# Kernel optimization log

Hardware: AMD Instinct MI355X
Metric: run time of the kernel (lower is better)

The kernel has to match this reference:

```python
import jax, jax.numpy as jnp
import numpy as np

B, L = 2, 2048
DIM, VOCAB, NL = 1024, 32000, 4
DSTATE, DCONV, EXPAND, HEADDIM = 128, 4, 2, 64
DIN = EXPAND * DIM            # 2048
H = DIN // HEADDIM            # 32 heads
CONVDIM = DIN + 2 * DSTATE    # 2304
DPROJ = 2 * DIN + 2 * DSTATE + H  # 4384
FFN = 4 * DIM                 # 4096
Q = 128                       # SSD chunk size
EPS = 1e-6


def _rms(x):
    return x * jax.lax.rsqrt(jnp.mean(x * x, axis=-1, keepdims=True) + EPS)


def _causal_conv(x, w, b):
    # x [B,L,C], depthwise causal conv, w [C,DCONV], b [C]
    y = jax.lax.conv_general_dilated(
        x.transpose(0, 2, 1), w[:, None, :], (1,), [(DCONV - 1, 0)],
        dimension_numbers=('NCH', 'OIH', 'NCH'), feature_group_count=CONVDIM)
    return (y + b[:, None]).transpose(0, 2, 1)


def _ssd(x, dt, A, Bm, Cm):
    # Exact selective scan h_t = h_{t-1}*exp(dt_t*A) + dt_t * x_t B_t ; y_t = C_t . h_t
    # computed in chunked (SSD) matmul form. x [b,l,h,p], dt [b,l,h], A [h], Bm/Cm [b,l,n]
    b, l, h, p = x.shape
    n = Bm.shape[-1]
    c = l // Q
    xr = x.reshape(b, c, Q, h, p)
    dtr = dt.reshape(b, c, Q, h)
    ar = (dt * A).reshape(b, c, Q, h)          # per-step log-decay (<= 0)
    Br = Bm.reshape(b, c, Q, n)
    Cr = Cm.reshape(b, c, Q, n)
    ca = jnp.cumsum(ar, axis=2)                # inclusive cumulative log-decay
    # ---- intra-chunk: causal decay-weighted 'attention' ----
    cah = ca.transpose(0, 1, 3, 2)             # [b,c,h,Q]
    idx = jnp.arange(Q)
    mask = idx[:, None] >= idx[None, :]
    diff = jnp.where(mask[None, None, None], cah[..., :, None] - cah[..., None, :], -jnp.inf)
    M = jnp.exp(diff)                          # [b,c,h,Q,Q]
    CB = jnp.einsum('bcin,bcjn->bcij', Cr, Br)
    T = CB[:, :, None] * M                     # [b,c,h,Q,Q]
    y_intra = jnp.einsum('bchij,bcjh,bcjhp->bcihp', T, dtr, xr)
    # ---- chunk-final states ----
    w = jnp.exp(ca[:, :, -1:, :] - ca) * dtr   # [b,c,Q,h]
    states = jnp.einsum('bcjh,bcjn,bcjhp->bchpn', w, Br, xr)
    chunk_decay = jnp.exp(ca[:, :, -1, :])     # [b,c,h]
    def step(s, inp):
        cd, st = inp
        prev = s
        s = s * cd[:, :, None, None] + st
        return s, prev
    s0 = jnp.zeros((b, h, p, n), x.dtype)
    _, s_prev = jax.lax.scan(step, s0, (chunk_decay.transpose(1, 0, 2),
                                        states.transpose(1, 0, 2, 3, 4)))
    s_prev = s_prev.transpose(1, 0, 2, 3, 4)   # [b,c,h,p,n] state entering each chunk
    y_inter = jnp.einsum('bcih,bcin,bchpn->bcihp', jnp.exp(ca), Cr, s_prev)
    return (y_intra + y_inter).reshape(b, l, h, p)


def _mamba(x, Wi, cw, cb, dtb, Alog, Dp, nw, Wo):
    bsz, sl, _ = x.shape
    zxbcdt = x @ Wi.T                          # [b,l,DPROJ]
    z = zxbcdt[..., :DIN]
    xBC = zxbcdt[..., DIN:DIN + CONVDIM]
    dtraw = zxbcdt[..., DIN + CONVDIM:]
    xBC = jax.nn.silu(_causal_conv(xBC, cw, cb))
    xs = xBC[..., :DIN]
    Bm = xBC[..., DIN:DIN + DSTATE]
    Cm = xBC[..., DIN + DSTATE:]
    dt = jax.nn.softplus(dtraw + dtb)
    A = -jnp.exp(Alog)
    x4 = xs.reshape(bsz, sl, H, HEADDIM)
    y = _ssd(x4, dt, A, Bm, Cm) + Dp[None, None, :, None] * x4
    y = y.reshape(bsz, sl, DIN)
    yg = y * jax.nn.silu(z)                    # gated RMSNorm (norm_before_gate=False)
    y = _rms(yg) * nw
    return y @ Wo.T


def _forward(tokens, embedding, lm_head_bias, in_proj_w, conv_w, conv_b,
             dt_bias, A_log, D, mnorm_w, out_proj_w, u_w, v_w, o_w):
    x = embedding[tokens]
    for li in range(NL):
        for _ in range(2):  # original applies each (mamba, ffn) pair twice
            x = _rms(x)
            x = x + _mamba(x, in_proj_w[li], conv_w[li], conv_b[li], dt_bias[li],
                           A_log[li], D[li], mnorm_w[li], out_proj_w[li])
            x = _rms(x)
            x = x + ((x @ u_w[li].T) * (x @ v_w[li].T)) @ o_w[li].T  # SGLU, dropout=0
    return x @ embedding.T + lm_head_bias      # tied lm_head


def setup_inputs():
    key = jax.random.key(0)
    ks = jax.random.split(key, 16)
    s = 0.02
    return {
        'tokens': jax.random.randint(ks[0], (B, L), 0, VOCAB),
        'embedding': jax.random.normal(ks[1], (VOCAB, DIM), jnp.float32) * s,
        'lm_head_bias': jnp.zeros((VOCAB,), jnp.float32),
        'in_proj_w': jax.random.normal(ks[2], (NL, DPROJ, DIM), jnp.float32) * s,
        'conv_w': jax.random.normal(ks[3], (NL, CONVDIM, DCONV), jnp.float32) * 0.2,
        'conv_b': jnp.zeros((NL, CONVDIM), jnp.float32),
        'dt_bias': jax.random.normal(ks[4], (NL, H), jnp.float32) * 0.3 - 3.0,
        'A_log': jnp.log(jax.random.uniform(ks[5], (NL, H), jnp.float32, 1.0, 16.0)),
        'D': jnp.ones((NL, H), jnp.float32) + 0.1 * jax.random.normal(ks[6], (NL, H), jnp.float32),
        'mnorm_w': jnp.ones((NL, DIN), jnp.float32),
        'out_proj_w': jax.random.normal(ks[7], (NL, DIM, DIN), jnp.float32) * s,
        'u_w': jax.random.normal(ks[8], (NL, FFN, DIM), jnp.float32) * s,
        'v_w': jax.random.normal(ks[9], (NL, FFN, DIM), jnp.float32) * s,
        'o_w': jax.random.normal(ks[10], (NL, DIM, FFN), jnp.float32) * s,
    }


def reference(tokens, embedding, lm_head_bias, in_proj_w, conv_w, conv_b,
              dt_bias, A_log, D, mnorm_w, out_proj_w, u_w, v_w, o_w):
    return _forward(tokens, embedding, lm_head_bias, in_proj_w, conv_w, conv_b,
                    dt_bias, A_log, D, mnorm_w, out_proj_w, u_w, v_w, o_w)
```

## Files before the change

### kernel.cpp

```cpp
#include <hip/hip_runtime.h>
#include <hip/hip_bf16.h>

#define BSZ 2
#define LSEQ 2048
#define DIM 1024
#define VOCAB 32000
#define NLAYER 4
#define DSTATE 128
#define DCONV 4
#define HEADDIM 64
#define DIN 2048
#define NH 32
#define CONVDIM 2304
#define DPROJ 4384
#define FFN 4096
#define QLEN 128
#define NTOK 4096
#define NCHUNK 32
#define CPB 16
#define DTOFF 4352

#define SMEM_BYTES 147456
#define SMEM2 131072

using f32x4 = __attribute__((ext_vector_type(4))) float;
using f16   = _Float16;
using f16x4 = __attribute__((ext_vector_type(4))) _Float16;
using f16x8 = __attribute__((ext_vector_type(8))) _Float16;

__device__ __forceinline__ void gld16(const void* g, void* l) {
  __builtin_amdgcn_global_load_lds(
      (const __attribute__((address_space(1))) unsigned int*)g,
      (__attribute__((address_space(3))) unsigned int*)l, 16, 0, 0);
}

__device__ __forceinline__ void swz_tiles(int& bx, int& by) {
  const int nx = gridDim.x, ny = gridDim.y;
  const int nwg = nx * ny;
  int bid = blockIdx.y * nx + blockIdx.x;
  if ((nwg & 7) == 0) bid = (bid & 7) * (nwg >> 3) + (bid >> 3);
  const int CW = 8;
  const int nchx = nx / CW;
  const int per = CW * ny;
  const int ch = bid / per;
  if (ch < nchx) {
    int wi = bid - ch * per;
    bx = ch * CW + (wi & (CW - 1));
    by = wi / CW;
  } else {
    int tb = bid - nchx * per;
    int tw = nx - nchx * CW;
    bx = nchx * CW + (tb % tw);
    by = tb / tw;
  }
}

__global__ __launch_bounds__(512, 2) void gemm_p(
    const f16* __restrict__ A, const f16* __restrict__ B,
    f16* __restrict__ Cg, float* __restrict__ dtr,
    int N, int Ksub, int lda, int ldb, int ldc)
{
  extern __shared__ char smem[];
  const int tid  = threadIdx.x;
  const int lane = tid & 63;
  const int wid  = tid >> 6;
  int bx, by; swz_tiles(bx, by);
  const int m0 = by * 256;
  const int n0 = bx * 128;
  const size_t kbase = (size_t)blockIdx.z * Ksub;
  if (gridDim.z > 1) Cg += (size_t)blockIdx.z * (size_t)gridDim.y * 256 * ldc;
  const int NT = Ksub >> 6;

  int arA[4], acA[4];
#pragma unroll
  for (int L = 0; L < 4; ++L) {
    int q = L * 512 + tid;
    int row = q >> 3;
    arA[L] = m0 + row;
    acA[L] = ((q & 7) ^ (row & 7)) << 3;
  }
  int brB[2], bcB[2];
#pragma unroll
  for (int L = 0; L < 2; ++L) {
    int q = L * 512 + tid;
    int row = q >> 3;
    int r = n0 + row; if (r > N - 1) r = N - 1;
    brB[L] = r;
    bcB[L] = ((q & 7) ^ (row & 7)) << 3;
  }

  auto stage = [&](int tt) {
    const int b = tt - (tt / 3) * 3;
    char* Ad = smem + b * 32768;
    char* Bd = smem + 98304 + b * 16384;
    const int kb = tt << 6;
#pragma unroll
    for (int L = 0; L < 4; ++L)
      gld16(A + (size_t)arA[L] * lda + kbase + kb + acA[L], Ad + (L * 512 + tid) * 16);
#pragma unroll
    for (int L = 0; L < 2; ++L)
      gld16(B + (size_t)brB[L] * ldb + kbase + kb + bcB[L], Bd + (L * 512 + tid) * 16);
  };

  const int wm = (wid >> 1) << 6;
  const int wn = (wid & 1) << 6;
  const int fr = lane & 15;
  const int kg = lane >> 4;

  f32x4 acc[4][4] = {};

  stage(0);
  stage(1);

  for (int t = 0; t < NT; ++t) {
    const int b = t - (t / 3) * 3;
    if (t + 2 < NT) {
      stage(t + 2);
      asm volatile("s_waitcnt vmcnt(12)" ::: "memory");
    } else if (t + 1 < NT) {
      asm volatile("s_waitcnt vmcnt(6)" ::: "memory");
    } else {
      asm volatile("s_waitcnt vmcnt(0)" ::: "memory");
    }
    __builtin_amdgcn_s_barrier();
    asm volatile("" ::: "memory");
    const f16* Ab = (const f16*)(smem + b * 32768);
    const f16* Bb = (const f16*)(smem + 98304 + b * 16384);
#pragma unroll
    for (int s = 0; s < 2; ++s) {
      f16x8 af[4], bf[4];
#pragma unroll
      for (int j = 0; j < 4; ++j) {
        int row = wm + j * 16 + fr;
        int g = kg + s * 4;
        af[j] = *(const f16x8*)&Ab[row * 64 + ((g ^ (row & 7)) << 3)];
      }
#pragma unroll
      for (int i = 0; i < 4; ++i) {
        int row = wn + i * 16 + fr;
        int g = kg + s * 4;
        bf[i] = *(const f16x8*)&Bb[row * 64 + ((g ^ (row & 7)) << 3)];
      }
      __builtin_amdgcn_s_setprio(1);
#pragma unroll
      for (int i = 0; i < 4; ++i)
#pragma unroll
        for (int j = 0; j < 4; ++j)
          acc[i][j] = __builtin_amdgcn_mfma_f32_16x16x32_f16(bf[i], af[j], acc[i][j], 0, 0, 0);
      __builtin_amdgcn_s_setprio(0);
    }
    asm volatile("" ::: "memory");
    __builtin_amdgcn_s_barrier();
    asm volatile("" ::: "memory");
  }

  const int c4 = kg << 2;
#pragma unroll
  for (int i = 0; i < 4; ++i) {
    const int col = n0 + wn + i * 16 + c4;
    if (col >= N) continue;
#pragma unroll
    for (int j = 0; j < 4; ++j) {
      const int row = m0 + wm + j * 16 + fr;
      f16x4 h;
#pragma unroll
      for (int r = 0; r < 4; ++r) h[r] = (f16)acc[i][j][r];
      *(f16x4*)(Cg + (size_t)row * ldc + col) = h;
      if (dtr && col >= DTOFF)
        *(f32x4*)(dtr + (size_t)row * NH + (col - DTOFF)) = acc[i][j];
    }
  }
}

__global__ __launch_bounds__(512, 2) void gemm_p2(
    const f16* __restrict__ A, const f16* __restrict__ B,
    float* __restrict__ Cf, const float* __restrict__ bias,
    int N, int Ksub, int lda, int ldb, int ldc)
{
  extern __shared__ char smem[];
  const int tid  = threadIdx.x;
  const int lane = tid & 63;
  const int wid  = tid >> 6;
  int bx, by; swz_tiles(bx, by);
  const int m0 = by * 256;
  const int n0 = bx * 256;
  const size_t kbase = (size_t)blockIdx.z * Ksub;
  const int NT = Ksub >> 6;

  int arA[4], acA[4], brB[4], bcB[4];
#pragma unroll
  for (int L = 0; L < 4; ++L) {
    int q = L * 512 + tid;
    int row = q >> 3;
    arA[L] = m0 + row;
    acA[L] = ((q & 7) ^ (row & 7)) << 3;
    int r = n0 + row; if (r > N - 1) r = N - 1;
    brB[L] = r;
    bcB[L] = acA[L];
  }

  auto stage = [&](int tt) {
    const int b = tt & 1;
    char* Ad = smem + b * 65536;
    char* Bd = Ad + 32768;
    const int kb = tt << 6;
#pragma unroll
    for (int L = 0; L < 4; ++L)
      gld16(A + (size_t)arA[L] * lda + kbase + kb + acA[L], Ad + (L * 512 + tid) * 16);
#pragma unroll
    for (int L = 0; L < 4; ++L)
      gld16(B + (size_t)brB[L] * ldb + kbase + kb + bcB[L], Bd + (L * 512 + tid) * 16);
  };

  const int wm = (wid >> 2) << 7;
  const int wn = (wid & 3) << 6;
  const int fr = lane & 15;
  const int kg = lane >> 4;

  f32x4 acc[4][8] = {};

  stage(0);

  for (int t = 0; t < NT; ++t) {
    if (t + 1 < NT) {
      stage(t + 1);
      asm volatile("s_waitcnt vmcnt(8)" ::: "memory");
    } else {
      asm volatile("s_waitcnt vmcnt(0)" ::: "memory");
    }
    __builtin_amdgcn_s_barrier();
    asm volatile("" ::: "memory");
    const f16* Ab = (const f16*)(smem + (t & 1) * 65536);
    const f16* Bb = Ab + 16384;
#pragma unroll
    for (int s = 0; s < 2; ++s) {
      const int g = kg + s * 4;
      f16x8 af[8], bf[4];
#pragma unroll
      for (int j = 0; j < 8; ++j) {
        int row = wm + j * 16 + fr;
        af[j] = *(const f16x8*)&Ab[row * 64 + ((g ^ (row & 7)) << 3)];
      }
#pragma unroll
      for (int i = 0; i < 4; ++i) {
        int row = wn + i * 16 + fr;
        bf[i] = *(const f16x8*)&Bb[row * 64 + ((g ^ (row & 7)) << 3)];
      }
      __builtin_amdgcn_s_setprio(1);
#pragma unroll
      for (int i = 0; i < 4; ++i)
#pragma unroll
        for (int j = 0; j < 8; ++j)
          acc[i][j] = __builtin_amdgcn_mfma_f32_16x16x32_f16(bf[i], af[j], acc[i][j], 0, 0, 0);
      __builtin_amdgcn_s_setprio(0);
    }
    asm volatile("" ::: "memory");
    __builtin_amdgcn_s_barrier();
    asm volatile("" ::: "memory");
  }

  const int c4 = kg << 2;
#pragma unroll
  for (int i = 0; i < 4; ++i) {
    const int col = n0 + wn + i * 16 + c4;
    if (col >= N) continue;
    f32x4 bv = bias ? *(const f32x4*)(bias + col) : f32x4{0, 0, 0, 0};
#pragma unroll
    for (int j = 0; j < 8; ++j) {
      const int row = m0 + wm + j * 16 + fr;
      *(f32x4*)(Cf + (size_t)row * ldc + col) = acc[i][j] + bv;
    }
  }
}

__global__ __launch_bounds__(512, 2) void gemm_uv2(
    const f16* __restrict__ A, const f16* __restrict__ Bu, const f16* __restrict__ Bv,
    f16* __restrict__ Gh)
{
  extern __shared__ char smem[];
  const int tid  = threadIdx.x;
  const int lane = tid & 63;
  const int wid  = tid >> 6;
  int bx, by; swz_tiles(bx, by);
  const int m0 = by * 256;
  const int n0 = bx * 128;
  const int NT = DIM >> 6;

  int arA[4], acA[4];
  const f16* bp[4];
  int bcB[4];
#pragma unroll
  for (int L = 0; L < 4; ++L) {
    int q = L * 512 + tid;
    int row = q >> 3;
    arA[L] = m0 + row;
    acA[L] = ((q & 7) ^ (row & 7)) << 3;
    bcB[L] = acA[L];
    bp[L] = (row < 128) ? (Bu + (size_t)(n0 + row) * DIM)
                        : (Bv + (size_t)(n0 + row - 128) * DIM);
  }

  auto stage = [&](int tt) {
    const int b = tt & 1;
    char* Ad = smem + b * 65536;
    char* Bd = Ad + 32768;
    const int kb = tt << 6;
#pragma unroll
    for (int L = 0; L < 4; ++L)
      gld16(A + (size_t)arA[L] * DIM + kb + acA[L], Ad + (L * 512 + tid) * 16);
#pragma unroll
    for (int L = 0; L < 4; ++L)
      gld16(bp[L] + kb + bcB[L], Bd + (L * 512 + tid) * 16);
  };

  const int wm = (wid >> 1) << 6;
  const int wn = (wid & 1) << 6;
  const int fr = lane & 15;
  const int kg = lane >> 4;

  f32x4 accu[4][4] = {}, accv[4][4] = {};

  stage(0);

  for (int t = 0; t < NT; ++t) {
    if (t + 1 < NT) {
      stage(t + 1);
      asm volatile("s_waitcnt vmcnt(8)" ::: "memory");
    } else {
      asm volatile("s_waitcnt vmcnt(0)" ::: "memory");
    }
    __builtin_amdgcn_s_barrier();
    asm volatile("" ::: "memory");
    const f16* Ab = (const f16*)(smem + (t & 1) * 65536);
    const f16* Bb = Ab + 16384;
#pragma unroll
    for (int s = 0; s < 2; ++s) {
      const int g = kg + s * 4;
      f16x8 af[4], bfu[4], bfv[4];
#pragma unroll
      for (int j = 0; j < 4; ++j) {
        int row = wm + j * 16 + fr;
        af[j] = *(const f16x8*)&Ab[row * 64 + ((g ^ (row & 7)) << 3)];
      }
#pragma unroll
      for (int i = 0; i < 4; ++i) {
        int ru = wn + i * 16 + fr;
        int rv = 128 + wn + i * 16 + fr;
        bfu[i] = *(const f16x8*)&Bb[ru * 64 + ((g ^ (ru & 7)) << 3)];
        bfv[i] = *(const f16x8*)&Bb[rv * 64 + ((g ^ (rv & 7)) << 3)];
      }
      __builtin_amdgcn_s_setprio(1);
#pragma unroll
      for (int i = 0; i < 4; ++i)
#pragma unroll
        for (int j = 0; j < 4; ++j) {
          accu[i][j] = __builtin_amdgcn_mfma_f32_16x16x32_f16(bfu[i], af[j], accu[i][j], 0, 0, 0);
          accv[i][j] = __builtin_amdgcn_mfma_f32_16x16x32_f16(bfv[i], af[j], accv[i][j], 0, 0, 0);
        }
      __builtin_amdgcn_s_setprio(0);
    }
    asm volatile("" ::: "memory");
    __builtin_amdgcn_s_barrier();
    asm volatile("" ::: "memory");
  }

  const int c4 = kg << 2;
#pragma unroll
  for (int i = 0; i < 4; ++i) {
    const int col = n0 + wn + i * 16 + c4;
#pragma unroll
    for (int j = 0; j < 4; ++j) {
      const int row = m0 + wm + j * 16 + fr;
      f16x4 h;
#pragma unroll
      for (int r = 0; r < 4; ++r)
        h[r] = (f16)(accu[i][j][r] * accv[i][j][r]);
      *(f16x4*)(Gh + (size_t)row * FFN + col) = h;
    }
  }
}

template <bool DORMS>
__global__ __launch_bounds__(256) void reduce_rms(const f16* __restrict__ parts,
                                                  const float* __restrict__ resid,
                                                  float* __restrict__ xn,
                                                  f16* __restrict__ outh, int np)
{
  const int row = blockIdx.x, tid = threadIdx.x;
  const size_t base = (size_t)row * DIM + tid * 4;
  f32x4 s = *(const f32x4*)(resid + base);
  for (int p = 0; p < np; ++p) {
    f16x4 pv = *(const f16x4*)(parts + (size_t)p * (NTOK * DIM) + base);
#pragma unroll
    for (int c = 0; c < 4; ++c) s[c] += (float)pv[c];
  }
  if constexpr (!DORMS) {
    f16x4 h;
#pragma unroll
    for (int c = 0; c < 4; ++c) h[c] = (f16)s[c];
    *(f16x4*)(outh + base) = h;
    return;
  }
  float ss = s[0] * s[0] + s[1] * s[1] + s[2] * s[2] + s[3] * s[3];
  for (int o = 32; o; o >>= 1) ss += __shfl_down(ss, o);
  __shared__ float red[4];
  if ((tid & 63) == 0) red[tid >> 6] = ss;
  __syncthreads();
  ss = red[0] + red[1] + red[2] + red[3];
  const float sc = rsqrtf(ss * (1.f / 1024.f) + 1e-6f);
  f32x4 o4 = s * sc;
  *(f32x4*)(xn + base) = o4;
  f16x4 h;
#pragma unroll
  for (int c = 0; c < 4; ++c) h[c] = (f16)o4[c];
  *(f16x4*)(outh + base) = h;
}

__global__ __launch_bounds__(256) void cvt_f2h_k(const float* __restrict__ src,
                                                 f16* __restrict__ dst, int n)
{
  for (size_t i = ((size_t)blockIdx.x * 256 + threadIdx.x) * 4; i < (size_t)n;
       i += (size_t)gridDim.x * 1024) {
    f32x4 v = *(const f32x4*)(src + i);
    f16x4 o;
#pragma unroll
    for (int c = 0; c < 4; ++c) o[c] = (f16)v[c];
    *(f16x4*)(dst + i) = o;
  }
}

__global__ __launch_bounds__(256) void cvt_wts(
    const float* __restrict__ inw, const float* __restrict__ outw,
    const float* __restrict__ uw, const float* __restrict__ vw,
    const float* __restrict__ ow,
    f16* __restrict__ w_in, f16* __restrict__ w_out,
    f16* __restrict__ w_uv, f16* __restrict__ w_o)
{
  const int b = blockIdx.x;
  const float* src; f16* dst;
  if (b < 17536) {
    int li = b / 4384, ib = b - li * 4384;
    src = inw  + (size_t)li * 4489216 + (size_t)ib * 1024;
    dst = w_in + (size_t)li * 4489216 + (size_t)ib * 1024;
  } else if (b < 25728) {
    int lb = b - 17536, li = lb >> 11, ib = lb & 2047;
    src = outw  + (size_t)li * 2097152 + (size_t)ib * 1024;
    dst = w_out + (size_t)li * 2097152 + (size_t)ib * 1024;
  } else if (b < 42112) {
    int lb = b - 25728, li = lb >> 12, ib = lb & 4095;
    src = uw   + (size_t)li * 4194304 + (size_t)ib * 1024;
    dst = w_uv + (size_t)li * 8388608 + (size_t)ib * 1024;
  } else if (b < 58496) {
    int lb = b - 42112, li = lb >> 12, ib = lb & 4095;
    src = vw   + (size_t)li * 4194304 + (size_t)ib * 1024;
    dst = w_uv + (size_t)li * 8388608 + 4194304 + (size_t)ib * 1024;
  } else {
    int lb = b - 58496, li = lb >> 12, ib = lb & 4095;
    src = ow  + (size_t)li * 4194304 + (size_t)ib * 1024;
    dst = w_o + (size_t)li * 4194304 + (size_t)ib * 1024;
  }
  const size_t i = (size_t)threadIdx.x * 4;
  f32x4 v = *(const f32x4*)(src + i);
  f16x4 o;
#pragma unroll
  for (int c = 0; c < 4; ++c) o[c] = (f16)v[c];
  *(f16x4*)(dst + i) = o;
}

__global__ __launch_bounds__(256) void gather_k(const int* __restrict__ tok,
                                                const float* __restrict__ emb,
                                                float* __restrict__ x)
{
  const int row = blockIdx.x;
  const int t = tok[row];
  const f32x4* s = (const f32x4*)(emb + (size_t)t * DIM);
  f32x4* d = (f32x4*)(x + (size_t)row * DIM);
  d[threadIdx.x] = s[threadIdx.x];
}

__global__ __launch_bounds__(256) void rms1024(const float* __restrict__ in,
                                               float* __restrict__ outf,
                                               f16* __restrict__ outh)
{
  const int row = blockIdx.x, tid = threadIdx.x;
  f32x4 v = ((const f32x4*)(in + (size_t)row * DIM))[tid];
  float ss = v[0] * v[0] + v[1] * v[1] + v[2] * v[2] + v[3] * v[3];
  for (int o = 32; o; o >>= 1) ss += __shfl_down(ss, o);
  __shared__ float red[4];
  if ((tid & 63) == 0) red[tid >> 6] = ss;
  __syncthreads();
  ss = red[0] + red[1] + red[2] + red[3];
  const float sc = rsqrtf(ss * (1.f / 1024.f) + 1e-6f);
  f32x4 o4 = v * sc;
  ((f32x4*)(outf + (size_t)row * DIM))[tid] = o4;
  f16x4 h;
#pragma unroll
  for (int c = 0; c < 4; ++c) h[c] = (f16)o4[c];
  ((f16x4*)(outh + (size_t)row * DIM))[tid] = h;
}

__global__ __launch_bounds__(256) void convdt(const f16* __restrict__ zx,
                                              const float* __restrict__ dtrw,
                                              const float* __restrict__ cw,
                                              const float* __restrict__ cbias,
                                              const float* __restrict__ dtb,
                                              const float* __restrict__ alog,
                                              f16* __restrict__ xbc,
                                              float* __restrict__ dt,
                                              float* __restrict__ ca)
{
  if (blockIdx.x < 576) {
    const int sid = blockIdx.x * 256 + threadIdx.x;
    const int c0 = (sid % 576) * 4;
    const int t0 = (sid / 576) * 16;
    float w[4][4], bs[4];
#pragma unroll
    for (int cc = 0; cc < 4; ++cc) {
      f32x4 wv = *(const f32x4*)(cw + (size_t)(c0 + cc) * 4);
      w[cc][0] = wv[0]; w[cc][1] = wv[1]; w[cc][2] = wv[2]; w[cc][3] = wv[3];
      bs[cc] = cbias[c0 + cc];
    }
    const int l0 = t0 & (LSEQ - 1);
    float x3[4] = {}, x2[4] = {}, x1[4] = {};
    if (l0 != 0) {
      f16x4 a = *(const f16x4*)(zx + (size_t)(t0 - 3) * DPROJ + DIN + c0);
      f16x4 b = *(const f16x4*)(zx + (size_t)(t0 - 2) * DPROJ + DIN + c0);
      f16x4 d = *(const f16x4*)(zx + (size_t)(t0 - 1) * DPROJ + DIN + c0);
#pragma unroll
      for (int c = 0; c < 4; ++c) { x3[c] = (float)a[c]; x2[c] = (float)b[c]; x1[c] = (float)d[c]; }
    }
    for (int i = 0; i < 16; ++i) {
      const int t = t0 + i;
      f16x4 xcv = *(const f16x4*)(zx + (size_t)t * DPROJ + DIN + c0);
      f16x4 o;
#pragma unroll
      for (int cc = 0; cc < 4; ++cc) {
        float xc = (float)xcv[cc];
        float a = bs[cc] + x3[cc] * w[cc][0] + x2[cc] * w[cc][1] +
                  x1[cc] * w[cc][2] + xc * w[cc][3];
        o[cc] = (f16)(a / (1.f + expf(-a)));
        x3[cc] = x2[cc]; x2[cc] = x1[cc]; x1[cc] = xc;
      }
      *(f16x4*)(xbc + (size_t)t * CONVDIM + c0) = o;
    }
  } else {
    const int loc = (threadIdx.x >> 7) * 128;
    const int u = (blockIdx.x - 576) * 2 + (threadIdx.x >> 7);
    const int bc = u >> 5, h = u & 31, q = threadIdx.x & 127;
    const int t = bc * 128 + q;
    float raw = dtrw[(size_t)t * NH + h] + dtb[h];
    float d = raw > 20.f ? raw : log1pf(expf(raw));
    dt[t * 32 + h] = d;
    float a = -expf(alog[h]) * d;
    __shared__ float s[256];
    s[loc + q] = a;
    __syncthreads();
    for (int off = 1; off < 128; off <<= 1) {
      float v = (q >= off) ? s[loc + q - off] : 0.f;
      __syncthreads();
      s[loc + q] += v;
      __syncthreads();
    }
    ca[(size_t)u * 128 + q] = s[loc + q];
  }
}

__global__ __launch_bounds__(256) void cb_mfma(const f16* __restrict__ xbc,
                                               float* __restrict__ CBo)
{
  const int bc = blockIdx.x;
  __shared__ f16 Cm[128 * 72], Bm[128 * 72];
  const int tid = threadIdx.x, lane = tid & 63, wid = tid >> 6;
  const int fr = lane & 15, kg = lane >> 4;
  f32x4 acc[2][8] = {};
  const int i = tid & 127;
  const f16* rowp = xbc + (size_t)(bc * 128 + i) * CONVDIM + DIN;

  for (int kh = 0; kh < 2; ++kh) {
#pragma unroll
    for (int it = 0; it < 8; ++it) {
      int idx = it * 256 + tid;
      int n0 = (idx >> 7) * 4;
      *(f16x4*)&Bm[i * 72 + n0] = *(const f16x4*)(rowp + kh * 64 + n0);
      *(f16x4*)&Cm[i * 72 + n0] = *(const f16x4*)(rowp + DSTATE + kh * 64 + n0);
    }
    __syncthreads();
#pragma unroll
    for (int kf = 0; kf < 2; ++kf) {
      const int ko = kf * 32 + kg * 8;
      f16x8 cf[2], bf[8];
#pragma unroll
      for (int ii = 0; ii < 2; ++ii)
        cf[ii] = *(const f16x8*)&Cm[((wid * 2 + ii) * 16 + fr) * 72 + ko];
#pragma unroll
      for (int jj = 0; jj < 8; ++jj)
        bf[jj] = *(const f16x8*)&Bm[(jj * 16 + fr) * 72 + ko];
      __builtin_amdgcn_s_setprio(1);
#pragma unroll
      for (int ii = 0; ii < 2; ++ii)
#pragma unroll
        for (int jj = 0; jj < 8; ++jj)
          acc[ii][jj] = __builtin_amdgcn_mfma_f32_16x16x32_f16(cf[ii], bf[jj], acc[ii][jj], 0, 0, 0);
      __builtin_amdgcn_s_setprio(0);
    }
    __syncthreads();
  }
  float* out = CBo + (size_t)bc * 16384;
#pragma unroll
  for (int ii = 0; ii < 2; ++ii) {
    const int i0 = (wid * 2 + ii) * 16 + kg * 4;
#pragma unroll
    for (int jj = 0; jj < 8; ++jj) {
      const int j = jj * 16 + fr;
#pragma unroll
      for (int r = 0; r < 4; ++r)
        out[(size_t)(i0 + r) * 128 + j] = acc[ii][jj][r];
    }
  }
}

__global__ __launch_bounds__(256) void ssd_states(const f16* __restrict__ xbc,
                                                  const float* __restrict__ dt,
                                                  const float* __restrict__ ca,
                                                  float* __restrict__ ST)
{
  const int bc = blockIdx.x >> 5, h = blockIdx.x & 31;
  __shared__ f16 Am[128 * 136];
  __shared__ f16 Bm[64 * 136];
  __shared__ float warr[128];
  const int tid = threadIdx.x, lane = tid & 63, wid = tid >> 6;
  if (tid < 128) {
    float cv = ca[(size_t)blockIdx.x * 128 + tid];
    float cl = ca[(size_t)blockIdx.x * 128 + 127];
    warr[tid] = expf(cl - cv) * dt[(size_t)(bc * 128 + tid) * 32 + h];
  }
  __syncthreads();
  {
    const int j = tid & 127;
    const float wj = warr[j];
    const f16* br = xbc + (size_t)(bc * 128 + j) * CONVDIM + DIN;
#pragma unroll
    for (int it = 0; it < 16; ++it) {
      int idx = it * 256 + tid;
      int n0 = (idx >> 7) * 4;
      f16x4 v = *(const f16x4*)(br + n0);
#pragma unroll
      for (int c = 0; c < 4; ++c) Am[(n0 + c) * 136 + j] = (f16)((float)v[c] * wj);
    }
    const f16* xr = xbc + (size_t)(bc * 128 + j) * CONVDIM + h * 64;
#pragma unroll
    for (int it = 0; it < 8; ++it) {
      int idx = it * 256 + tid;
      int p0 = (idx >> 7) * 4;
      f16x4 v = *(const f16x4*)(xr + p0);
#pragma unroll
      for (int c = 0; c < 4; ++c) Bm[(p0 + c) * 136 + j] = v[c];
    }
  }
  __syncthreads();
  const int fr = lane & 15, kg = lane >> 4;
  f32x4 acc[2][4] = {};
#pragma unroll
  for (int kf = 0; kf < 4; ++kf) {
    const int ko = kf * 32 + kg * 8;
    f16x8 bw[2], xf[4];
#pragma unroll
    for (int ii = 0; ii < 2; ++ii)
      bw[ii] = *(const f16x8*)&Am[((wid * 2 + ii) * 16 + fr) * 136 + ko];
#pragma unroll
    for (int pi = 0; pi < 4; ++pi)
      xf[pi] = *(const f16x8*)&Bm[(pi * 16 + fr) * 136 + ko];
    __builtin_amdgcn_s_setprio(1);
#pragma unroll
    for (int ii = 0; ii < 2; ++ii)
#pragma unroll
      for (int pi = 0; pi < 4; ++pi)
        acc[ii][pi] = __builtin_amdgcn_mfma_f32_16x16x32_f16(bw[ii], xf[pi], acc[ii][pi], 0, 0, 0);
    __builtin_amdgcn_s_setprio(0);
  }
  float* sb = ST + (size_t)blockIdx.x * 8192;
#pragma unroll
  for (int ii = 0; ii < 2; ++ii) {
    const int n0 = (wid * 2 + ii) * 16 + kg * 4;
#pragma unroll
    for (int pi = 0; pi < 4; ++pi) {
      const int p = pi * 16 + fr;
      *(f32x4*)(sb + (size_t)p * 128 + n0) = acc[ii][pi];
    }
  }
}

__global__ __launch_bounds__(256) void scan_k(const float* __restrict__ ca,
                                              float* __restrict__ states)
{
  const int b = blockIdx.x >> 10, h = (blockIdx.x >> 5) & 31, seg = blockIdx.x & 31;
  const int e = seg * 256 + threadIdx.x;
  float s = 0.f;
  for (int c = 0; c < CPB; ++c) {
    int bc = b * CPB + c;
    float cd = expf(ca[(size_t)(bc * 32 + h) * 128 + 127]);
    size_t idx = (size_t)(bc * 32 + h) * 8192 + e;
    float v = states[idx];
    states[idx] = s;
    s = s * cd + v;
  }
}

__global__ __launch_bounds__(256) void ssd_y(const f16* __restrict__ xbc,
                                             const float* __restrict__ dt,
                                             const float* __restrict__ ca,
                                             const float* __restrict__ CB,
                                             const float* __restrict__ Dvec,
                                             const float* __restrict__ ST,
                                             f16* __restrict__ ybuf)
{
  const int bc = blockIdx.x >> 5, h = blockIdx.x & 31;
  __shared__ f16 Am[128 * 136];
  __shared__ f16 Bm[64 * 136];
  __shared__ float cas[128], dtl[128];
  const int tid = threadIdx.x, lane = tid & 63, wid = tid >> 6;
  if (tid < 128) {
    cas[tid] = ca[(size_t)blockIdx.x * 128 + tid];
    dtl[tid] = dt[(size_t)(bc * 128 + tid) * 32 + h];
  }
  __syncthreads();
  {
    const int j = tid & 127;
    const float dj = dtl[j];
    const f16* xr = xbc + (size_t)(bc * 128 + j) * CONVDIM + h * 64;
#pragma unroll
    for (int it = 0; it < 8; ++it) {
      int idx = it * 256 + tid;
      int p0 = (idx >> 7) * 4;
      f16x4 v = *(const f16x4*)(xr + p0);
#pragma unroll
      for (int c = 0; c < 4; ++c) Bm[(p0 + c) * 136 + j] = (f16)((float)v[c] * dj);
    }
  }
  {
    const int i = tid >> 1;
    const int jh = (tid & 1) * 64;
    const float cai = cas[i];
    const float* cbr = CB + (size_t)bc * 16384 + (size_t)i * 128 + jh;
#pragma unroll
    for (int g = 0; g < 8; ++g) {
      int j0 = g * 8;
      f32x4 v0 = *(const f32x4*)(cbr + j0);
      f32x4 v1 = *(const f32x4*)(cbr + j0 + 4);
      f16x8 tv;
#pragma unroll
      for (int c = 0; c < 8; ++c) {
        int j = jh + j0 + c;
        float cbv = (c < 4) ? v0[c] : v1[c - 4];
        float val = (j <= i) ? cbv * expf(cai - cas[j]) : 0.f;
        tv[c] = (f16)val;
      }
      *(f16x8*)&Am[i * 136 + jh + j0] = tv;
    }
  }
  __syncthreads();
  const int fr = lane & 15, kg = lane >> 4;
  f32x4 a1[2][4] = {}, a2[2][4] = {};
#pragma unroll
  for (int kf = 0; kf < 4; ++kf) {
    const int ko = kf * 32 + kg * 8;
    f16x8 xf[4], tf[2];
#pragma unroll
    for (int pi = 0; pi < 4; ++pi)
      xf[pi] = *(const f16x8*)&Bm[(pi * 16 + fr) * 136 + ko];
#pragma unroll
    for (int ii = 0; ii < 2; ++ii)
      tf[ii] = *(const f16x8*)&Am[((wid * 2 + ii) * 16 + fr) * 136 + ko];
    __builtin_amdgcn_s_setprio(1);
#pragma unroll
    for (int ii = 0; ii < 2; ++ii)
#pragma unroll
      for (int pi = 0; pi < 4; ++pi)
        a1[ii][pi] = __builtin_amdgcn_mfma_f32_16x16x32_f16(xf[pi], tf[ii], a1[ii][pi], 0, 0, 0);
    __builtin_amdgcn_s_setprio(0);
  }
  __syncthreads();
  {
    const int i = tid & 127;
    const f16* cr = xbc + (size_t)(bc * 128 + i) * CONVDIM + DIN + DSTATE;
#pragma unroll
    for (int it = 0; it < 16; ++it) {
      int idx = it * 256 + tid;
      int n0 = (idx >> 7) * 4;
      *(f16x4*)&Am[i * 136 + n0] = *(const f16x4*)(cr + n0);
    }
    const float* sr = ST + (size_t)blockIdx.x * 8192;
    const int p = tid & 63;
#pragma unroll
    for (int it = 0; it < 8; ++it) {
      int idx = it * 256 + tid;
      int n0 = (idx >> 6) * 4;
      f32x4 v = *(const f32x4*)(sr + (size_t)p * 128 + n0);
      f16x4 hv;
#pragma unroll
      for (int c = 0; c < 4; ++c) hv[c] = (f16)v[c];
      *(f16x4*)&Bm[p * 136 + n0] = hv;
    }
  }
  __syncthreads();
#pragma unroll
  for (int kf = 0; kf < 4; ++kf) {
    const int ko = kf * 32 + kg * 8;
    f16x8 sf[4], cf[2];
#pragma unroll
    for (int pi = 0; pi < 4; ++pi)
      sf[pi] = *(const f16x8*)&Bm[(pi * 16 + fr) * 136 + ko];
#pragma unroll
    for (int ii = 0; ii < 2; ++ii)
      cf[ii] = *(const f16x8*)&Am[((wid * 2 + ii) * 16 + fr) * 136 + ko];
    __builtin_amdgcn_s_setprio(1);
#pragma unroll
    for (int ii = 0; ii < 2; ++ii)
#pragma unroll
      for (int pi = 0; pi < 4; ++pi)
        a2[ii][pi] = __builtin_amdgcn_mfma_f32_16x16x32_f16(sf[pi], cf[ii], a2[ii][pi], 0, 0, 0);
    __builtin_amdgcn_s_setprio(0);
  }
  const float dh = Dvec[h];
#pragma unroll
  for (int ii = 0; ii < 2; ++ii) {
    const int i = (wid * 2 + ii) * 16 + fr;
    const float ei = expf(cas[i]);
    const int tg = bc * 128 + i;
#pragma unroll
    for (int pi = 0; pi < 4; ++pi) {
      const int p0 = pi * 16 + kg * 4;
      f16x4 xv = *(const f16x4*)(xbc + (size_t)tg * CONVDIM + h * 64 + p0);
      f16x4 yo;
#pragma unroll
      for (int r = 0; r < 4; ++r)
        yo[r] = (f16)(a1[ii][pi][r] + ei * a2[ii][pi][r] + dh * (float)xv[r]);
      *(f16x4*)(ybuf + (size_t)tg * DIN + h * 64 + p0) = yo;
    }
  }
}

__global__ __launch_bounds__(256) void gate_rms(const f16* __restrict__ ybuf,
                                                const f16* __restrict__ zx,
                                                const float* __restrict__ nw,
                                                f16* __restrict__ outh)
{
  const int row = blockIdx.x, tid = threadIdx.x;
  f16x8 yv = *(const f16x8*)(ybuf + (size_t)row * DIN + tid * 8);
  f16x8 zv = *(const f16x8*)(zx + (size_t)row * DPROJ + tid * 8);
  float g[8];
  float ss = 0.f;
#pragma unroll
  for (int c = 0; c < 8; ++c) {
    float z = (float)zv[c];
    g[c] = (float)yv[c] * (z / (1.f + expf(-z)));
    ss += g[c] * g[c];
  }
  for (int o = 32; o; o >>= 1) ss += __shfl_down(ss, o);
  __shared__ float red[4];
  if ((tid & 63) == 0) red[tid >> 6] = ss;
  __syncthreads();
  ss = red[0] + red[1] + red[2] + red[3];
  const float sc = rsqrtf(ss * (1.f / 2048.f) + 1e-6f);
  f32x4 w0 = *(const f32x4*)(nw + tid * 8);
  f32x4 w1 = *(const f32x4*)(nw + tid * 8 + 4);
  f16x8 h;
#pragma unroll
  for (int c = 0; c < 8; ++c) {
    float w = (c < 4) ? w0[c] : w1[c - 4];
    h[c] = (f16)(g[c] * sc * w);
  }
  *(f16x8*)(outh + (size_t)row * DIN + tid * 8) = h;
}

extern "C" void kernel_launch(void* const* d_in, const int* in_sizes, int n_in,
                              void* d_out, int out_size, void* d_ws, size_t ws_size,
                              hipStream_t stream)
{
  (void)in_sizes; (void)n_in; (void)out_size; (void)ws_size;
  const int*   tokens = (const int*)d_in[0];
  const float* emb    = (const float*)d_in[1];
  const float* lmb    = (const float*)d_in[2];
  const float* inw    = (const float*)d_in[3];
  const float* cw     = (const float*)d_in[4];
  const float* cbias  = (const float*)d_in[5];
  const float* dtb    = (const float*)d_in[6];
  const float* alog   = (const float*)d_in[7];
  const float* Dvec   = (const float*)d_in[8];
  const float* nw     = (const float*)d_in[9];
  const float* outw   = (const float*)d_in[10];
  const float* uw     = (const float*)d_in[11];
  const float* vw     = (const float*)d_in[12];
  const float* ow     = (const float*)d_in[13];

  char* ws = (char*)d_ws;
  size_t off = 0;
  auto alloc = [&](size_t bytes) { void* p = ws + off; off += (bytes + 255) & ~(size_t)255; return p; };
  f16* emb_h   = (f16*)alloc((size_t)VOCAB * DIM * 2);
  float* xbuf  = (float*)alloc((size_t)NTOK * DIM * 4);
  float* xn    = (float*)alloc((size_t)NTOK * DIM * 4);
  f16* xnh     = (f16*)alloc((size_t)NTOK * DIM * 2);
  f16* xh_lm   = (f16*)alloc((size_t)NTOK * DIM * 2);
  float* dtraw = (float*)alloc((size_t)NTOK * NH * 4);
  float* dtbuf = (float*)alloc((size_t)NTOK * NH * 4);
  float* cabuf = (float*)alloc((size_t)NCHUNK * NH * QLEN * 4);
  float* CBbuf = (float*)alloc((size_t)NCHUNK * QLEN * QLEN * 4);
  f16* abh     = (f16*)alloc((size_t)NTOK * FFN * 2);

  char* ob = (char*)d_out;
  float* states = (float*)(ob);
  f16* zxb      = (f16*)(ob + 40000000);
  f16* xbc      = (f16*)(ob + 80000000);
  f16* ybuf     = (f16*)(ob + 100000000);
  f16* parts    = (f16*)(ob + 120000000);
  f16* w_in     = (f16*)(ob + 160000000);
  f16* w_out    = (f16*)(ob + 196000000);
  f16* w_uv     = (f16*)(ob + 213000000);
  f16* w_o      = (f16*)(ob + 281000000);

  cvt_f2h_k<<<4096, 256, 0, stream>>>(emb, emb_h, VOCAB * DIM);
  cvt_wts<<<74880, 256, 0, stream>>>(inw, outw, uw, vw, ow, w_in, w_out, w_uv, w_o);
  gather_k<<<NTOK, 256, 0, stream>>>(tokens, emb, xbuf);
  rms1024<<<NTOK, 256, 0, stream>>>(xbuf, xn, xnh);

  for (int it = 0; it < 2 * NLAYER; ++it) {
    const int li = it >> 1;
    const f16* w_inL  = w_in  + (size_t)li * 4489216;
    const f16* w_outL = w_out + (size_t)li * 2097152;
    const f16* w_uL   = w_uv  + (size_t)li * 8388608;
    const f16* w_vL   = w_uL  + 4194304;
    const f16* w_oL   = w_o   + (size_t)li * 4194304;
    gemm_p<<<dim3((DPROJ + 127) / 128, NTOK / 256, 1), 512, SMEM_BYTES, stream>>>(
        xnh, w_inL, zxb, dtraw, DPROJ, DIM, DIM, DIM, DPROJ);
    convdt<<<1088, 256, 0, stream>>>(zxb, dtraw, cw + (size_t)li * CONVDIM * DCONV,
                                     cbias + (size_t)li * CONVDIM,
                                     dtb + li * NH, alog + li * NH, xbc, dtbuf, cabuf);
    cb_mfma<<<NCHUNK, 256, 0, stream>>>(xbc, CBbuf);
    ssd_states<<<NCHUNK * NH, 256, 0, stream>>>(xbc, dtbuf, cabuf, states);
    scan_k<<<2048, 256, 0, stream>>>(cabuf, states);
    ssd_y<<<NCHUNK * NH, 256, 0, stream>>>(xbc, dtbuf, cabuf, CBbuf,
                                           Dvec + li * NH, states, ybuf);
    gate_rms<<<NTOK, 256, 0, stream>>>(ybuf, zxb, nw + (size_t)li * DIN, abh);
    gemm_p<<<dim3(DIM / 128, NTOK / 256, 2), 512, SMEM_BYTES, stream>>>(
        abh, w_outL, parts, nullptr, DIM, DIN / 2, DIN, DIN, DIM);
    reduce_rms<true><<<NTOK, 256, 0, stream>>>(parts, xn, xn, xnh, 2);
    gemm_uv2<<<dim3(FFN / 128, NTOK / 256, 1), 512, SMEM2, stream>>>(
        xnh, w_uL, w_vL, abh);
    gemm_p<<<dim3(DIM / 128, NTOK / 256, 2), 512, SMEM_BYTES, stream>>>(
        abh, w_oL, parts, nullptr, DIM, FFN / 2, FFN, FFN, DIM);
    if (it < 2 * NLAYER - 1)
      reduce_rms<true><<<NTOK, 256, 0, stream>>>(parts, xn, xn, xnh, 2);
    else
      reduce_rms<false><<<NTOK, 256, 0, stream>>>(parts, xn, nullptr, xh_lm, 2);
  }

  gemm_p2<<<dim3(VOCAB / 256, NTOK / 256, 1), 512, SMEM2, stream>>>(
      xh_lm, emb_h, (float*)d_out, lmb, VOCAB, DIM, DIM, DIM, VOCAB);
}
```

Measured before the change: 3.165 ms.

## Use one barrier per k-step in gemm_p and reuse it for LM head

```diff
diff --git a/kernel.cpp b/kernel.cpp
--- a/kernel.cpp
+++ b/kernel.cpp
@@ -55,9 +55,11 @@
   }
 }
 
+template <int MODE>
 __global__ __launch_bounds__(512, 2) void gemm_p(
     const f16* __restrict__ A, const f16* __restrict__ B,
-    f16* __restrict__ Cg, float* __restrict__ dtr,
+    f16* __restrict__ Cg, float* __restrict__ Cf,
+    float* __restrict__ dtr, const float* __restrict__ bias,
     int N, int Ksub, int lda, int ldb, int ldc)
 {
   extern __shared__ char smem[];
@@ -114,16 +116,14 @@
 
   for (int t = 0; t < NT; ++t) {
     const int b = t - (t / 3) * 3;
-    if (t + 2 < NT) {
-      stage(t + 2);
-      asm volatile("s_waitcnt vmcnt(12)" ::: "memory");
-    } else if (t + 1 < NT) {
+    if (t + 1 < NT) {
       asm volatile("s_waitcnt vmcnt(6)" ::: "memory");
     } else {
       asm volatile("s_waitcnt vmcnt(0)" ::: "memory");
     }
     __builtin_amdgcn_s_barrier();
     asm volatile("" ::: "memory");
+    if (t + 2 < NT) stage(t + 2);
     const f16* Ab = (const f16*)(smem + b * 32768);
     const f16* Bb = (const f16*)(smem + 98304 + b * 16384);
 #pragma unroll
@@ -150,8 +150,6 @@
       __builtin_amdgcn_s_setprio(0);
     }
     asm volatile("" ::: "memory");
-    __builtin_amdgcn_s_barrier();
-    asm volatile("" ::: "memory");
   }
 
   const int c4 = kg << 2;
@@ -162,113 +160,17 @@
 #pragma unroll
     for (int j = 0; j < 4; ++j) {
       const int row = m0 + wm + j * 16 + fr;
-      f16x4 h;
-#pragma unroll
-      for (int r = 0; r < 4; ++r) h[r] = (f16)acc[i][j][r];
-      *(f16x4*)(Cg + (size_t)row * ldc + col) = h;
-      if (dtr && col >= DTOFF)
-        *(f32x4*)(dtr + (size_t)row * NH + (col - DTOFF)) = acc[i][j];
-    }
-  }
-}
-
-__global__ __launch_bounds__(512, 2) void gemm_p2(
-    const f16* __restrict__ A, const f16* __restrict__ B,
-    float* __restrict__ Cf, const float* __restrict__ bias,
-    int N, int Ksub, int lda, int ldb, int ldc)
-{
-  extern __shared__ char smem[];
-  const int tid  = threadIdx.x;
-  const int lane = tid & 63;
-  const int wid  = tid >> 6;
-  int bx, by; swz_tiles(bx, by);
-  const int m0 = by * 256;
-  const int n0 = bx * 256;
-  const size_t kbase = (size_t)blockIdx.z * Ksub;
-  const int NT = Ksub >> 6;
-
-  int arA[4], acA[4], brB[4], bcB[4];
-#pragma unroll
-  for (int L = 0; L < 4; ++L) {
-    int q = L * 512 + tid;
-    int row = q >> 3;
-    arA[L] = m0 + row;
-    acA[L] = ((q & 7) ^ (row & 7)) << 3;
-    int r = n0 + row; if (r > N - 1) r = N - 1;
-    brB[L] = r;
-    bcB[L] = acA[L];
-  }
-
-  auto stage = [&](int tt) {
-    const int b = tt & 1;
-    char* Ad = smem + b * 65536;
-    char* Bd = Ad + 32768;
-    const int kb = tt << 6;
-#pragma unroll
-    for (int L = 0; L < 4; ++L)
-      gld16(A + (size_t)arA[L] * lda + kbase + kb + acA[L], Ad + (L * 512 + tid) * 16);
-#pragma unroll
-    for (int L = 0; L < 4; ++L)
-      gld16(B + (size_t)brB[L] * ldb + kbase + kb + bcB[L], Bd + (L * 512 + tid) * 16);
-  };
-
-  const int wm = (wid >> 2) << 7;
-  const int wn = (wid & 3) << 6;
-  const int fr = lane & 15;
-  const int kg = lane >> 4;
-
-  f32x4 acc[4][8] = {};
-
-  stage(0);
-
-  for (int t = 0; t < NT; ++t) {
-    if (t + 1 < NT) {
-      stage(t + 1);
-      asm volatile("s_waitcnt vmcnt(8)" ::: "memory");
-    } else {
-      asm volatile("s_waitcnt vmcnt(0)" ::: "memory");
-    }
-    __builtin_amdgcn_s_barrier();
-    asm volatile("" ::: "memory");
-    const f16* Ab = (const f16*)(smem + (t & 1) * 65536);
-    const f16* Bb = Ab + 16384;
-#pragma unroll
-    for (int s = 0; s < 2; ++s) {
-      const int g = kg + s * 4;
-      f16x8 af[8], bf[4];
-#pragma unroll
-      for (int j = 0; j < 8; ++j) {
-        int row = wm + j * 16 + fr;
-        af[j] = *(const f16x8*)&Ab[row * 64 + ((g ^ (row & 7)) << 3)];
+      if constexpr (MODE == 1) {
+        f32x4 bv = bias ? *(const f32x4*)(bias + col) : f32x4{0, 0, 0, 0};
+        *(f32x4*)(Cf + (size_t)row * ldc + col) = acc[i][j] + bv;
+      } else {
+        f16x4 h;
+#pragma unroll
+        for (int r = 0; r < 4; ++r) h[r] = (f16)acc[i][j][r];
+        *(f16x4*)(Cg + (size_t)row * ldc + col) = h;
+        if (dtr && col >= DTOFF)
+          *(f32x4*)(dtr + (size_t)row * NH + (col - DTOFF)) = acc[i][j];
       }
-#pragma unroll
-      for (int i = 0; i < 4; ++i) {
-        int row = wn + i * 16 + fr;
-        bf[i] = *(const f16x8*)&Bb[row * 64 + ((g ^ (row & 7)) << 3)];
-      }
-      __builtin_amdgcn_s_setprio(1);
-#pragma unroll
-      for (int i = 0; i < 4; ++i)
-#pragma unroll
-        for (int j = 0; j < 8; ++j)
-          acc[i][j] = __builtin_amdgcn_mfma_f32_16x16x32_f16(bf[i], af[j], acc[i][j], 0, 0, 0);
-      __builtin_amdgcn_s_setprio(0);
-    }
-    asm volatile("" ::: "memory");
-    __builtin_amdgcn_s_barrier();
-    asm volatile("" ::: "memory");
-  }
-
-  const int c4 = kg << 2;
-#pragma unroll
-  for (int i = 0; i < 4; ++i) {
-    const int col = n0 + wn + i * 16 + c4;
-    if (col >= N) continue;
-    f32x4 bv = bias ? *(const f32x4*)(bias + col) : f32x4{0, 0, 0, 0};
-#pragma unroll
-    for (int j = 0; j < 8; ++j) {
-      const int row = m0 + wm + j * 16 + fr;
-      *(f32x4*)(Cf + (size_t)row * ldc + col) = acc[i][j] + bv;
     }
   }
 }
@@ -930,8 +832,8 @@
     const f16* w_uL   = w_uv  + (size_t)li * 8388608;
     const f16* w_vL   = w_uL  + 4194304;
     const f16* w_oL   = w_o   + (size_t)li * 4194304;
-    gemm_p<<<dim3((DPROJ + 127) / 128, NTOK / 256, 1), 512, SMEM_BYTES, stream>>>(
-        xnh, w_inL, zxb, dtraw, DPROJ, DIM, DIM, DIM, DPROJ);
+    gemm_p<0><<<dim3((DPROJ + 127) / 128, NTOK / 256, 1), 512, SMEM_BYTES, stream>>>(
+        xnh, w_inL, zxb, nullptr, dtraw, nullptr, DPROJ, DIM, DIM, DIM, DPROJ);
     convdt<<<1088, 256, 0, stream>>>(zxb, dtraw, cw + (size_t)li * CONVDIM * DCONV,
                                      cbias + (size_t)li * CONVDIM,
                                      dtb + li * NH, alog + li * NH, xbc, dtbuf, cabuf);
@@ -941,19 +843,19 @@
     ssd_y<<<NCHUNK * NH, 256, 0, stream>>>(xbc, dtbuf, cabuf, CBbuf,
                                            Dvec + li * NH, states, ybuf);
     gate_rms<<<NTOK, 256, 0, stream>>>(ybuf, zxb, nw + (size_t)li * DIN, abh);
-    gemm_p<<<dim3(DIM / 128, NTOK / 256, 2), 512, SMEM_BYTES, stream>>>(
-        abh, w_outL, parts, nullptr, DIM, DIN / 2, DIN, DIN, DIM);
+    gemm_p<0><<<dim3(DIM / 128, NTOK / 256, 2), 512, SMEM_BYTES, stream>>>(
+        abh, w_outL, parts, nullptr, nullptr, nullptr, DIM, DIN / 2, DIN, DIN, DIM);
     reduce_rms<true><<<NTOK, 256, 0, stream>>>(parts, xn, xn, xnh, 2);
     gemm_uv2<<<dim3(FFN / 128, NTOK / 256, 1), 512, SMEM2, stream>>>(
         xnh, w_uL, w_vL, abh);
-    gemm_p<<<dim3(DIM / 128, NTOK / 256, 2), 512, SMEM_BYTES, stream>>>(
-        abh, w_oL, parts, nullptr, DIM, FFN / 2, FFN, FFN, DIM);
+    gemm_p<0><<<dim3(DIM / 128, NTOK / 256, 2), 512, SMEM_BYTES, stream>>>(
+        abh, w_oL, parts, nullptr, nullptr, nullptr, DIM, FFN / 2, FFN, FFN, DIM);
     if (it < 2 * NLAYER - 1)
       reduce_rms<true><<<NTOK, 256, 0, stream>>>(parts, xn, xn, xnh, 2);
     else
       reduce_rms<false><<<NTOK, 256, 0, stream>>>(parts, xn, nullptr, xh_lm, 2);
   }
 
-  gemm_p2<<<dim3(VOCAB / 256, NTOK / 256, 1), 512, SMEM2, stream>>>(
-      xh_lm, emb_h, (float*)d_out, lmb, VOCAB, DIM, DIM, DIM, VOCAB);
-}
+  gemm_p<1><<<dim3(VOCAB / 128, NTOK / 256, 1), 512, SMEM_BYTES, stream>>>(
+      xh_lm, emb_h, nullptr, (float*)d_out, nullptr, lmb, VOCAB, DIM, DIM, DIM, VOCAB);
+}
```

Result: faster. 3.084 ms (-2.5%).
